# Kernel tuning notes

Hardware: AMD Instinct MI355X
Metric: run time of the kernel (lower is better)

Reference implementation:

```python
import jax, jax.numpy as jnp
import numpy as np

EPS = 1e-15
BALL_EPS = 1e-5  # geoopt-style clamp away from the ball boundary


def expmap0(u):
    # Poincare ball (curvature -1): expmap0(u) = tanh(||u||) * u / ||u||
    n = jnp.linalg.norm(u, axis=-1, keepdims=True)
    n = jnp.maximum(n, EPS)
    return jnp.tanh(n) * u / n


def setup_inputs() -> dict:
    key = jax.random.key(0)
    k1, k2, k3 = jax.random.split(key, 3)
    B, H, D, L = 32768, 768, 384, 128
    cls_output = jax.random.normal(k1, (B, H), dtype=jnp.float32)
    W_proj = jax.random.normal(k2, (H, D), dtype=jnp.float32) * 0.02
    b_proj = jnp.zeros((D,), dtype=jnp.float32)
    # class prototypes: uniform(-0.1, 0.1) then expmap0, as in __init__
    tangent = jax.random.uniform(k3, (L, D), dtype=jnp.float32, minval=-0.1, maxval=0.1)
    poincare_weight = expmap0(tangent)
    return {"cls_output": cls_output, "W_proj": W_proj, "b_proj": b_proj,
            "poincare_weight": poincare_weight}


def reference(cls_output, W_proj, b_proj, poincare_weight):
    # projection (dropout is identity in eval mode)
    projected = cls_output @ W_proj + b_proj            # [B, D]
    x = expmap0(projected)                              # [B, D] points in ball
    y = poincare_weight                                 # [L, D] class reps in ball
    # Poincare distance for all (B, L) pairs, fused via dot products:
    # ||(-x) mobius+ y||^2 = ||x - y||^2 / (1 - 2<x,y> + ||x||^2 ||y||^2)
    x2 = jnp.sum(x * x, axis=-1)                        # [B]
    y2 = jnp.sum(y * y, axis=-1)                        # [L]
    xy = x @ y.T                                        # [B, L]
    sq_diff = x2[:, None] + y2[None, :] - 2.0 * xy      # ||x - y||^2
    denom = 1.0 - 2.0 * xy + x2[:, None] * y2[None, :]
    ratio = jnp.clip(sq_diff / denom, 0.0, (1.0 - BALL_EPS) ** 2)
    dist = 2.0 * jnp.arctanh(jnp.sqrt(ratio))           # [B, L]
    logits = -dist
    return logits, x
```

## Files before the change

kernel.cpp:

```cpp
#include <hip/hip_runtime.h>

typedef __attribute__((ext_vector_type(8))) short bf16x8;
typedef __attribute__((ext_vector_type(16))) float f32x16;

__device__ __forceinline__ unsigned short f2b(float f) {
  unsigned x = __builtin_bit_cast(unsigned, f);
  x += 0x7fffu + ((x >> 16) & 1u);
  return (unsigned short)(x >> 16);
}

__device__ __forceinline__ void dma16(const unsigned short* g, unsigned short* l) {
  __builtin_amdgcn_global_load_lds(
      (const __attribute__((address_space(1))) unsigned int*)g,
      (__attribute__((address_space(3))) unsigned int*)l, 16, 0, 0);
}

__global__ __launch_bounds__(256) void k_prep(const float* __restrict__ W,
                                              const float* __restrict__ Y,
                                              unsigned short* __restrict__ Wt,
                                              unsigned short* __restrict__ Ybf,
                                              float* __restrict__ y2) {
  int b = blockIdx.x;
  if (b < 144) {
    int fid = b * 256 + threadIdx.x;
    int kt  = fid / 3072;
    int rem = fid - kt * 3072;
    int sh  = rem / 384;
    int n   = rem - sh * 384;
    const float* src = W + (size_t)(kt * 64 + sh * 8) * 384 + n;
    unsigned short o[8];
#pragma unroll
    for (int i = 0; i < 8; i++) o[i] = f2b(src[(size_t)i * 384]);
    uint4 p;
    p.x = (unsigned)o[0] | ((unsigned)o[1] << 16);
    p.y = (unsigned)o[2] | ((unsigned)o[3] << 16);
    p.z = (unsigned)o[4] | ((unsigned)o[5] << 16);
    p.w = (unsigned)o[6] | ((unsigned)o[7] << 16);
    *(uint4*)(Wt + (size_t)fid * 8) = p;
  } else {
    int t = threadIdx.x;
    for (int i = t; i < 12288; i += 256) {
      float4 v = ((const float4*)Y)[i];
      ushort4 o;
      o.x = f2b(v.x); o.y = f2b(v.y); o.z = f2b(v.z); o.w = f2b(v.w);
      ((ushort4*)Ybf)[i] = o;
    }
    if (t < 128) {
      const float4* row = (const float4*)(Y + (size_t)t * 384);
      float s = 0.f;
#pragma unroll
      for (int j = 0; j < 96; j++) {
        float4 v = row[j];
        s += v.x * v.x + v.y * v.y + v.z * v.z + v.w * v.w;
      }
      y2[t] = s;
    }
  }
}

#define LDSA 72
#define LDSX 392

__global__ __launch_bounds__(1024, 4) void k_main(const float* __restrict__ cls,
                                                  const unsigned short* __restrict__ Wt,
                                                  const float* __restrict__ bias,
                                                  const unsigned short* __restrict__ Ybf,
                                                  const float* __restrict__ y2,
                                                  float* __restrict__ xout,
                                                  float* __restrict__ out) {
  __shared__ __align__(16) unsigned short sm[67584];
  __shared__ float rs[128][4];
  __shared__ float sF[128];
  __shared__ float sQ[128];

  const int tid = threadIdx.x;
  const int bm = blockIdx.x * 128;
  const int wave = tid >> 6, lane = tid & 63;
  const int r = lane & 31, h = lane >> 5;
  const int rg = wave & 3, cg = wave >> 2;

  f32x16 acc[3];
#pragma unroll
  for (int j = 0; j < 3; j++)
#pragma unroll
    for (int e = 0; e < 16; e++) acc[j][e] = 0.f;

  const int arow = tid >> 3, akc = tid & 7;
  const float* asrc = cls + (size_t)(bm + arow) * 768 + akc * 8;

  {
    unsigned short* wdst = sm + 18432;
    const unsigned short* wsrc = Wt;
#pragma unroll
    for (int i = 0; i < 3; i++) {
      int fb = (wave * 3 + i) * 64;
      dma16(wsrc + (size_t)(fb + lane) * 8, wdst + fb * 8);
    }
  }
  float4 rA[2][2];
  rA[0][0] = *(const float4*)(asrc);
  rA[0][1] = *(const float4*)(asrc + 4);
  rA[1][0] = *(const float4*)(asrc + 64);
  rA[1][1] = *(const float4*)(asrc + 68);

#pragma unroll
  for (int t = 0; t < 12; t++) {
    {
      uint4 p;
      p.x = (unsigned)f2b(rA[t & 1][0].x) | ((unsigned)f2b(rA[t & 1][0].y) << 16);
      p.y = (unsigned)f2b(rA[t & 1][0].z) | ((unsigned)f2b(rA[t & 1][0].w) << 16);
      p.z = (unsigned)f2b(rA[t & 1][1].x) | ((unsigned)f2b(rA[t & 1][1].y) << 16);
      p.w = (unsigned)f2b(rA[t & 1][1].z) | ((unsigned)f2b(rA[t & 1][1].w) << 16);
      *(uint4*)(sm + (t & 1) * 9216 + arow * LDSA + akc * 8) = p;
    }
    if (t < 11) asm volatile("s_waitcnt vmcnt(2) lgkmcnt(0)" ::: "memory");
    else        asm volatile("s_waitcnt vmcnt(0) lgkmcnt(0)" ::: "memory");
    __builtin_amdgcn_s_barrier();
    if (t + 1 < 12) {
      unsigned short* wdst = sm + 18432 + ((t + 1) & 1) * 24576;
      const unsigned short* wsrc = Wt + (size_t)(t + 1) * 3072 * 8;
#pragma unroll
      for (int i = 0; i < 3; i++) {
        int fb = (wave * 3 + i) * 64;
        dma16(wsrc + (size_t)(fb + lane) * 8, wdst + fb * 8);
      }
    }
    if (t + 2 < 12) {
      rA[t & 1][0] = *(const float4*)(asrc + (t + 2) * 64);
      rA[t & 1][1] = *(const float4*)(asrc + (t + 2) * 64 + 4);
    }
    const unsigned short* ab = sm + (t & 1) * 9216;
    const unsigned short* wb = sm + 18432 + (t & 1) * 24576;
#pragma unroll
    for (int s = 0; s < 4; s++) {
      bf16x8 a = *(const bf16x8*)(ab + (rg * 32 + r) * LDSA + s * 16 + h * 8);
      const unsigned short* wf = wb + (size_t)((s * 2 + h) * 384) * 8;
      bf16x8 b0 = *(const bf16x8*)(wf + (size_t)(cg * 96 + r) * 8);
      bf16x8 b1 = *(const bf16x8*)(wf + (size_t)(cg * 96 + 32 + r) * 8);
      bf16x8 b2 = *(const bf16x8*)(wf + (size_t)(cg * 96 + 64 + r) * 8);
      acc[0] = __builtin_amdgcn_mfma_f32_32x32x16_bf16(a, b0, acc[0], 0, 0, 0);
      acc[1] = __builtin_amdgcn_mfma_f32_32x32x16_bf16(a, b1, acc[1], 0, 0, 0);
      acc[2] = __builtin_amdgcn_mfma_f32_32x32x16_bf16(a, b2, acc[2], 0, 0, 0);
    }
  }

  float bcol[3];
#pragma unroll
  for (int j = 0; j < 3; j++) bcol[j] = bias[cg * 96 + j * 32 + r];

#pragma unroll
  for (int reg = 0; reg < 16; reg++) {
    float s = 0.f;
#pragma unroll
    for (int j = 0; j < 3; j++) {
      float v = acc[j][reg] + bcol[j];
      acc[j][reg] = v;
      s += v * v;
    }
    s += __shfl_xor(s, 1);
    s += __shfl_xor(s, 2);
    s += __shfl_xor(s, 4);
    s += __shfl_xor(s, 8);
    s += __shfl_xor(s, 16);
    if (r == 0) {
      int rowl = rg * 32 + (reg & 3) + 8 * (reg >> 2) + 4 * h;
      rs[rowl][cg] = s;
    }
  }
  asm volatile("s_waitcnt lgkmcnt(0)" ::: "memory");
  __builtin_amdgcn_s_barrier();
  if (tid < 128) {
    float n2 = rs[tid][0] + rs[tid][1] + rs[tid][2] + rs[tid][3];
    float n = fmaxf(sqrtf(n2), 1e-15f);
    float f = tanhf(n) / n;
    sF[tid] = f;
    sQ[tid] = n2 * f * f;
  }
  asm volatile("s_waitcnt lgkmcnt(0)" ::: "memory");
  __builtin_amdgcn_s_barrier();

#pragma unroll
  for (int reg = 0; reg < 16; reg++) {
    int rowl = rg * 32 + (reg & 3) + 8 * (reg >> 2) + 4 * h;
    float f = sF[rowl];
#pragma unroll
    for (int j = 0; j < 3; j++) {
      float v = acc[j][reg] * f;
      int col = cg * 96 + j * 32 + r;
      xout[(size_t)(bm + rowl) * 384 + col] = v;
      sm[rowl * LDSX + col] = f2b(v);
    }
  }
  asm volatile("s_waitcnt lgkmcnt(0)" ::: "memory");
  __builtin_amdgcn_s_barrier();

  const int rt = (wave & 3) * 32, ct = (wave >> 2) * 32;
  f32x16 acc2;
#pragma unroll
  for (int e = 0; e < 16; e++) acc2[e] = 0.f;

#pragma unroll
  for (int cc = 0; cc < 6; cc++) {
#pragma unroll
    for (int sub = 0; sub < 4; sub++) {
      const int kk = cc * 64 + sub * 16 + h * 8;
      bf16x8 a = *(const bf16x8*)(sm + (rt + r) * LDSX + kk);
      bf16x8 b = *(const bf16x8*)(Ybf + (size_t)(ct + r) * 384 + kk);
      acc2 = __builtin_amdgcn_mfma_f32_32x32x16_bf16(a, b, acc2, 0, 0, 0);
    }
  }

  const float CLIP = 0.9999800001f;
  float yc = y2[ct + r];
#pragma unroll
  for (int reg = 0; reg < 16; reg++) {
    int rowl = rt + (reg & 3) + 8 * (reg >> 2) + 4 * h;
    float xr = sQ[rowl];
    float xy = acc2[reg];
    float sq = xr + yc - 2.f * xy;
    float den = 1.f - 2.f * xy + xr * yc;
    float ratio = fminf(fmaxf(sq / den, 0.f), CLIP);
    float s = sqrtf(ratio);
    float dist = logf((1.f + s) / (1.f - s));
    out[(size_t)(bm + rowl) * 128 + ct + r] = -dist;
  }
}

extern "C" void kernel_launch(void* const* d_in, const int* in_sizes, int n_in,
                              void* d_out, int out_size, void* d_ws, size_t ws_size,
                              hipStream_t stream) {
  const float* cls  = (const float*)d_in[0];
  const float* W    = (const float*)d_in[1];
  const float* bias = (const float*)d_in[2];
  const float* Y    = (const float*)d_in[3];

  float* out_logits = (float*)d_out;
  float* out_x = out_logits + (size_t)32768 * 128;

  float* x2 = (float*)d_ws;
  float* y2 = x2 + 32768;
  unsigned short* Wt = (unsigned short*)(y2 + 128);
  unsigned short* Ybf = Wt + (size_t)384 * 768;

  k_prep<<<145, 256, 0, stream>>>(W, Y, Wt, Ybf, y2);
  k_main<<<256, 1024, 0, stream>>>(cls, Wt, bias, Ybf, y2, out_x, out_logits);
}
```

Before: 213.4 us.

## Halve row tile to 64 with 512 threads and single-buffer W tile

New measurement: 218.9 us. 1.03x slower.

```diff
diff --git a/kernel.cpp b/kernel.cpp
--- a/kernel.cpp
+++ b/kernel.cpp
@@ -61,23 +61,25 @@
 #define LDSA 72
 #define LDSX 392
 
-__global__ __launch_bounds__(1024, 4) void k_main(const float* __restrict__ cls,
-                                                  const unsigned short* __restrict__ Wt,
-                                                  const float* __restrict__ bias,
-                                                  const unsigned short* __restrict__ Ybf,
-                                                  const float* __restrict__ y2,
-                                                  float* __restrict__ xout,
-                                                  float* __restrict__ out) {
-  __shared__ __align__(16) unsigned short sm[67584];
-  __shared__ float rs[128][4];
-  __shared__ float sF[128];
-  __shared__ float sQ[128];
+__global__ __launch_bounds__(512, 4) void k_main(const float* __restrict__ cls,
+                                                 const unsigned short* __restrict__ Wt,
+                                                 const float* __restrict__ bias,
+                                                 const unsigned short* __restrict__ Ybf,
+                                                 const float* __restrict__ y2,
+                                                 float* __restrict__ xout,
+                                                 float* __restrict__ out) {
+  __shared__ __align__(16) unsigned short sm[33792];
+  __shared__ float rs[64][4];
+  __shared__ float sF[64];
+  __shared__ float sQ[64];
+
+  unsigned short* wb = sm + 9216;
 
   const int tid = threadIdx.x;
-  const int bm = blockIdx.x * 128;
+  const int bm = blockIdx.x * 64;
   const int wave = tid >> 6, lane = tid & 63;
   const int r = lane & 31, h = lane >> 5;
-  const int rg = wave & 3, cg = wave >> 2;
+  const int rg = wave & 1, cg = wave >> 1;
 
   f32x16 acc[3];
 #pragma unroll
@@ -88,59 +90,69 @@
   const int arow = tid >> 3, akc = tid & 7;
   const float* asrc = cls + (size_t)(bm + arow) * 768 + akc * 8;
 
-  {
-    unsigned short* wdst = sm + 18432;
-    const unsigned short* wsrc = Wt;
-#pragma unroll
-    for (int i = 0; i < 3; i++) {
-      int fb = (wave * 3 + i) * 64;
-      dma16(wsrc + (size_t)(fb + lane) * 8, wdst + fb * 8);
-    }
+#pragma unroll
+  for (int i = 0; i < 6; i++) {
+    int fb = (wave * 6 + i) * 64;
+    dma16(Wt + (size_t)(fb + lane) * 8, wb + (size_t)fb * 8);
   }
   float4 rA[2][2];
   rA[0][0] = *(const float4*)(asrc);
   rA[0][1] = *(const float4*)(asrc + 4);
   rA[1][0] = *(const float4*)(asrc + 64);
   rA[1][1] = *(const float4*)(asrc + 68);
+  {
+    uint4 p;
+    p.x = (unsigned)f2b(rA[0][0].x) | ((unsigned)f2b(rA[0][0].y) << 16);
+    p.y = (unsigned)f2b(rA[0][0].z) | ((unsigned)f2b(rA[0][0].w) << 16);
+    p.z = (unsigned)f2b(rA[0][1].x) | ((unsigned)f2b(rA[0][1].y) << 16);
+    p.w = (unsigned)f2b(rA[0][1].z) | ((unsigned)f2b(rA[0][1].w) << 16);
+    *(uint4*)(sm + arow * LDSA + akc * 8) = p;
+  }
 
 #pragma unroll
   for (int t = 0; t < 12; t++) {
-    {
-      uint4 p;
-      p.x = (unsigned)f2b(rA[t & 1][0].x) | ((unsigned)f2b(rA[t & 1][0].y) << 16);
-      p.y = (unsigned)f2b(rA[t & 1][0].z) | ((unsigned)f2b(rA[t & 1][0].w) << 16);
-      p.z = (unsigned)f2b(rA[t & 1][1].x) | ((unsigned)f2b(rA[t & 1][1].y) << 16);
-      p.w = (unsigned)f2b(rA[t & 1][1].z) | ((unsigned)f2b(rA[t & 1][1].w) << 16);
-      *(uint4*)(sm + (t & 1) * 9216 + arow * LDSA + akc * 8) = p;
-    }
     if (t < 11) asm volatile("s_waitcnt vmcnt(2) lgkmcnt(0)" ::: "memory");
     else        asm volatile("s_waitcnt vmcnt(0) lgkmcnt(0)" ::: "memory");
     __builtin_amdgcn_s_barrier();
+
+    {
+      const unsigned short* abt = sm + (t & 1) * 4608;
+#pragma unroll
+      for (int s = 0; s < 4; s++) {
+        bf16x8 a = *(const bf16x8*)(abt + (rg * 32 + r) * LDSA + s * 16 + h * 8);
+        const unsigned short* wf = wb + (size_t)((s * 2 + h) * 384) * 8;
+        bf16x8 b0 = *(const bf16x8*)(wf + (size_t)(cg * 96 + r) * 8);
+        bf16x8 b1 = *(const bf16x8*)(wf + (size_t)(cg * 96 + 32 + r) * 8);
+        bf16x8 b2 = *(const bf16x8*)(wf + (size_t)(cg * 96 + 64 + r) * 8);
+        acc[0] = __builtin_amdgcn_mfma_f32_32x32x16_bf16(a, b0, acc[0], 0, 0, 0);
+        acc[1] = __builtin_amdgcn_mfma_f32_32x32x16_bf16(a, b1, acc[1], 0, 0, 0);
+        acc[2] = __builtin_amdgcn_mfma_f32_32x32x16_bf16(a, b2, acc[2], 0, 0, 0);
+      }
+    }
+
     if (t + 1 < 12) {
-      unsigned short* wdst = sm + 18432 + ((t + 1) & 1) * 24576;
+      uint4 p;
+      p.x = (unsigned)f2b(rA[(t + 1) & 1][0].x) | ((unsigned)f2b(rA[(t + 1) & 1][0].y) << 16);
+      p.y = (unsigned)f2b(rA[(t + 1) & 1][0].z) | ((unsigned)f2b(rA[(t + 1) & 1][0].w) << 16);
+      p.z = (unsigned)f2b(rA[(t + 1) & 1][1].x) | ((unsigned)f2b(rA[(t + 1) & 1][1].y) << 16);
+      p.w = (unsigned)f2b(rA[(t + 1) & 1][1].z) | ((unsigned)f2b(rA[(t + 1) & 1][1].w) << 16);
+      *(uint4*)(sm + ((t + 1) & 1) * 4608 + arow * LDSA + akc * 8) = p;
+    }
+
+    asm volatile("s_waitcnt lgkmcnt(0)" ::: "memory");
+    __builtin_amdgcn_s_barrier();
+
+    if (t + 1 < 12) {
       const unsigned short* wsrc = Wt + (size_t)(t + 1) * 3072 * 8;
 #pragma unroll
-      for (int i = 0; i < 3; i++) {
-        int fb = (wave * 3 + i) * 64;
-        dma16(wsrc + (size_t)(fb + lane) * 8, wdst + fb * 8);
+      for (int i = 0; i < 6; i++) {
+        int fb = (wave * 6 + i) * 64;
+        dma16(wsrc + (size_t)(fb + lane) * 8, wb + (size_t)fb * 8);
       }
     }
     if (t + 2 < 12) {
       rA[t & 1][0] = *(const float4*)(asrc + (t + 2) * 64);
       rA[t & 1][1] = *(const float4*)(asrc + (t + 2) * 64 + 4);
-    }
-    const unsigned short* ab = sm + (t & 1) * 9216;
-    const unsigned short* wb = sm + 18432 + (t & 1) * 24576;
-#pragma unroll
-    for (int s = 0; s < 4; s++) {
-      bf16x8 a = *(const bf16x8*)(ab + (rg * 32 + r) * LDSA + s * 16 + h * 8);
-      const unsigned short* wf = wb + (size_t)((s * 2 + h) * 384) * 8;
-      bf16x8 b0 = *(const bf16x8*)(wf + (size_t)(cg * 96 + r) * 8);
-      bf16x8 b1 = *(const bf16x8*)(wf + (size_t)(cg * 96 + 32 + r) * 8);
-      bf16x8 b2 = *(const bf16x8*)(wf + (size_t)(cg * 96 + 64 + r) * 8);
-      acc[0] = __builtin_amdgcn_mfma_f32_32x32x16_bf16(a, b0, acc[0], 0, 0, 0);
-      acc[1] = __builtin_amdgcn_mfma_f32_32x32x16_bf16(a, b1, acc[1], 0, 0, 0);
-      acc[2] = __builtin_amdgcn_mfma_f32_32x32x16_bf16(a, b2, acc[2], 0, 0, 0);
     }
   }
 
@@ -169,7 +181,7 @@
   }
   asm volatile("s_waitcnt lgkmcnt(0)" ::: "memory");
   __builtin_amdgcn_s_barrier();
-  if (tid < 128) {
+  if (tid < 64) {
     float n2 = rs[tid][0] + rs[tid][1] + rs[tid][2] + rs[tid][3];
     float n = fmaxf(sqrtf(n2), 1e-15f);
     float f = tanhf(n) / n;
@@ -194,7 +206,7 @@
   asm volatile("s_waitcnt lgkmcnt(0)" ::: "memory");
   __builtin_amdgcn_s_barrier();
 
-  const int rt = (wave & 3) * 32, ct = (wave >> 2) * 32;
+  const int rt = (wave & 1) * 32, ct = (wave >> 1) * 32;
   f32x16 acc2;
 #pragma unroll
   for (int e = 0; e < 16; e++) acc2[e] = 0.f;
@@ -243,5 +255,5 @@
   unsigned short* Ybf = Wt + (size_t)384 * 768;
 
   k_prep<<<145, 256, 0, stream>>>(W, Y, Wt, Ybf, y2);
-  k_main<<<256, 1024, 0, stream>>>(cls, Wt, bias, Ybf, y2, out_x, out_logits);
-}
+  k_main<<<512, 512, 0, stream>>>(cls, Wt, bias, Ybf, y2, out_x, out_logits);
+}
```
